# Performance work log

Hardware: AMD Instinct MI355X
Metric: run time of the kernel (lower is better)

The kernel has to match this reference:

```python
import jax, jax.numpy as jnp
import numpy as np

# Dimensions inferred from the module (few-shot reweighted YOLOv2 region loss)
B, C, NA, NCPA = 64, 20, 5, 1          # batch, base classes, anchors, classes-per-anchor
H, W = 19, 19                           # feature map (608 input / stride 32)
T = 50                                  # cfg.max_boxes
THRESH = 0.6
COORD_SCALE = 1.0
CLASS_SCALE = 1.0
NB = B * C                              # per-class 'image' rows, as in the torch code
A4 = NA * H * W
EPS = 1e-12
BCE_EPS = 1e-7
ANCHORS = [[1.3221, 1.73145], [3.19275, 4.00944], [5.05587, 8.09892], [9.47112, 4.84053], [11.2364, 10.0071]]


def iou_xywh(x1, y1, w1, h1, x2, y2, w2, h2):
    # center-size IoU, matches darknet bbox_iou(x1y1x2y2=False)
    l = jnp.maximum(x1 - w1 * 0.5, x2 - w2 * 0.5)
    r = jnp.minimum(x1 + w1 * 0.5, x2 + w2 * 0.5)
    t = jnp.maximum(y1 - h1 * 0.5, y2 - h2 * 0.5)
    b = jnp.minimum(y1 + h1 * 0.5, y2 + h2 * 0.5)
    inter = jnp.clip(r - l, 0.0) * jnp.clip(b - t, 0.0)
    union = w1 * h1 + w2 * h2 - inter
    return inter / jnp.maximum(union, EPS)


def setup_inputs() -> dict:
    key = jax.random.key(0)
    k1, k2, k3, k4 = jax.random.split(key, 4)
    output = jax.random.normal(k1, (NB, NA * (5 + NCPA), H, W), jnp.float32) * 0.5
    # target rows: [cls, x, y, w, h] * T, coords in (0,1); x kept > 0 so all boxes are 'valid'
    cls_ids = jax.random.randint(k2, (B, C, T), 0, C).astype(jnp.float32)
    xy = jax.random.uniform(k3, (B, C, T, 2), minval=0.05, maxval=0.95)
    wh = jax.random.uniform(k4, (B, C, T, 2), minval=0.05, maxval=0.5)
    target = jnp.concatenate([cls_ids[..., None], xy, wh], axis=-1).reshape(B, C, T * 5)
    anchors = jnp.asarray(ANCHORS, jnp.float32)
    return {"output": output, "target": target, "anchors": anchors}


def _forward(output, target, anchors):
    target = jax.lax.stop_gradient(target)
    anchors = jax.lax.stop_gradient(anchors)
    out5 = output.reshape(NB, NA, 5 + NCPA, H, W)
    x = jax.nn.sigmoid(out5[:, :, 0])
    y = jax.nn.sigmoid(out5[:, :, 1])
    w = out5[:, :, 2]
    h = out5[:, :, 3]
    conf = jax.nn.sigmoid(out5[:, :, 4])
    # class logits regrouped to original batch: (B*NA*H*W, C)
    cls = out5[:, :, 5:5 + NCPA].reshape(NB, NA, H, W)
    cls_logits = cls.reshape(B, C, NA * H * W).transpose(0, 2, 1).reshape(-1, C)
    # decode pred boxes (detached, mirroring torch's use of .data)
    grid_x = jnp.arange(W, dtype=jnp.float32)[None, None, None, :]
    grid_y = jnp.arange(H, dtype=jnp.float32)[None, None, :, None]
    aw = anchors[:, 0][None, :, None, None]
    ah = anchors[:, 1][None, :, None, None]
    px = jax.lax.stop_gradient(x) + grid_x
    py = jax.lax.stop_gradient(y) + grid_y
    pw = jnp.exp(jax.lax.stop_gradient(w)) * aw
    ph = jnp.exp(jax.lax.stop_gradient(h)) * ah
    # ground-truth boxes per row
    tgt = target.reshape(NB, T, 5)
    cls_t = tgt[:, :, 0]
    gx = tgt[:, :, 1] * W
    gy = tgt[:, :, 2] * H
    gw = tgt[:, :, 3] * W
    gh = tgt[:, :, 4] * H
    # 'break on first zero x' semantics
    valid = jnp.cumprod((tgt[:, :, 1] != 0).astype(jnp.int32), axis=1) > 0
    # stage 1: zero conf_mask where any gt IoU > thresh (scan over T to avoid (NB,T,A4) blowup)
    pxf = px.reshape(NB, A4); pyf = py.reshape(NB, A4)
    pwf = pw.reshape(NB, A4); phf = ph.reshape(NB, A4)

    def iou_step(ci, xs):
        gxt, gyt, gwt, ght, vt = xs
        iou = iou_xywh(pxf, pyf, pwf, phf, gxt[:, None], gyt[:, None], gwt[:, None], ght[:, None])
        return jnp.maximum(ci, jnp.where(vt[:, None], iou, 0.0)), None

    cur_ious, _ = jax.lax.scan(iou_step, jnp.zeros((NB, A4), jnp.float32), (gx.T, gy.T, gw.T, gh.T, valid.T))
    conf_mask0 = jnp.where(cur_ious.reshape(NB, NA, H, W) > THRESH, 0.0, 1.0)
    # best anchor per gt by wh-only IoU
    inter = jnp.minimum(gw[..., None], anchors[:, 0]) * jnp.minimum(gh[..., None], anchors[:, 1])
    union = gw[..., None] * gh[..., None] + anchors[:, 0] * anchors[:, 1] - inter
    best_n = jnp.argmax(inter / jnp.maximum(union, EPS), axis=-1).astype(jnp.int32)  # (NB,T)
    gi = gx.astype(jnp.int32)
    gj = gy.astype(jnp.int32)
    # stage 2: ordered scatter of targets (later boxes overwrite earlier, as in the torch loops)
    binds = jnp.arange(NB)
    z = jnp.zeros((NB, NA, H, W), jnp.float32)
    # seen < 12800 branch: tx=ty=0.5, tw=th=0, coord_mask=1
    carry0 = (jnp.ones_like(z), z, conf_mask0, jnp.full_like(z, 0.5), jnp.full_like(z, 0.5), z, z, z, z)

    def tgt_step(carry, xs):
        cm, clm, cfm, tx, ty, tw, th, tconf, tcls = carry
        gxt, gyt, gwt, ght, bn, git, gjt, vt, ct = xs
        idx = (binds, bn, gjt, git)

        def upd(arr, val):
            return arr.at[idx].set(jnp.where(vt, val, arr[idx]))

        aw_b = anchors[bn, 0]
        ah_b = anchors[bn, 1]
        iou = iou_xywh(gxt, gyt, gwt, ght, px[idx], py[idx], pw[idx], ph[idx])
        cm = upd(cm, 1.0)
        clm = upd(clm, 1.0)
        cfm = upd(cfm, 1.0)
        tx = upd(tx, gxt - git.astype(jnp.float32))
        ty = upd(ty, gyt - gjt.astype(jnp.float32))
        tw = upd(tw, jnp.log(jnp.maximum(gwt, EPS) / aw_b))
        th = upd(th, jnp.log(jnp.maximum(ght, EPS) / ah_b))
        tconf = upd(tconf, iou)
        tcls = upd(tcls, ct)
        return (cm, clm, cfm, tx, ty, tw, th, tconf, tcls), None

    xs = (gx.T, gy.T, gw.T, gh.T, best_n.T, gi.T, gj.T, valid.T, cls_t.T)
    (coord_mask, cls_mask, conf_mask, tx, ty, tw, th, tconf, tcls), _ = jax.lax.scan(tgt_step, carry0, xs)
    # regroup per-class rows back to original batch (neg_ratio='full' -> counts[i] == C)
    cm_grp = cls_mask.reshape(B, C, NA, H, W).sum(axis=1)
    tcls_grp = tcls.reshape(B, C, NA, H, W).sum(axis=1)
    sel = (cm_grp == 1.0).reshape(-1)           # exclude colliding cells
    labels = tcls_grp.reshape(-1).astype(jnp.int32)

    def bce_mean(p, t):
        p = jnp.clip(p, BCE_EPS, 1.0 - BCE_EPS)
        return jnp.mean(-(t * jnp.log(p) + (1.0 - t) * jnp.log(1.0 - p)))

    loss_x = COORD_SCALE * bce_mean(x * coord_mask, tx * coord_mask)
    loss_y = COORD_SCALE * bce_mean(y * coord_mask, ty * coord_mask)
    loss_w = COORD_SCALE * 0.5 * jnp.mean((w * coord_mask - tw * coord_mask) ** 2)
    loss_h = COORD_SCALE * 0.5 * jnp.mean((h * coord_mask - th * coord_mask) ** 2)
    loss_conf = 0.5 * jnp.mean((conf * conf_mask - tconf * conf_mask) ** 2)
    logp = jax.nn.log_softmax(cls_logits, axis=-1)
    nll = -jnp.take_along_axis(logp, labels[:, None], axis=1)[:, 0]
    nsel = jnp.maximum(jnp.sum(sel.astype(jnp.float32)), 1.0)
    loss_cls = CLASS_SCALE * jnp.sum(jnp.where(sel, nll, 0.0)) / nsel
    return loss_x + loss_y + loss_w + loss_h + loss_conf + loss_cls


def reference(output, target, anchors):
    return _forward(output, target, anchors)
```

## Files before the change

kernel.cpp:

```cpp
#include <hip/hip_runtime.h>
#include <math.h>

constexpr int cB   = 64;
constexpr int cC   = 20;
constexpr int cNA  = 5;
constexpr int cH   = 19;
constexpr int cW   = 19;
constexpr int cT   = 50;
constexpr int cNB  = cB * cC;
constexpr int cHW  = cH * cW;
constexpr int cA4  = cNA * cHW;
constexpr int cCH  = cNA * 6;
constexpr long cNTOT = (long)cNB * cA4;
constexpr int cCLS_BLOCKS = cB * cNA * 2;

__device__ __constant__ float cAW[cNA]   = {1.3221f, 3.19275f, 5.05587f, 9.47112f, 11.2364f};
__device__ __constant__ float cAH[cNA]   = {1.73145f, 4.00944f, 8.09892f, 4.84053f, 10.0071f};
__device__ __constant__ float cAREA[cNA] = {2.28930345f, 12.80114796f, 40.94706183f, 45.84455262f, 112.44377644f};
__device__ __constant__ float cLNAW[cNA] = {0.27920469f, 1.16088088f, 1.62060702f, 2.24822684f, 2.41915174f};
__device__ __constant__ float cLNAH[cNA] = {0.54896100f, 1.38865236f, 2.09173157f, 1.57701337f, 2.30329495f};

constexpr int ACC_BANKS = 64;
constexpr size_t OFF_CNT = 2560;
constexpr size_t OFF_ROW = 4096;
constexpr size_t ZERO_BYTES = OFF_ROW + (size_t)cB * cA4 * 4;

__device__ __forceinline__ float fexp(float x) {
    return __builtin_amdgcn_exp2f(x * 1.4426950408889634f);
}
__device__ __forceinline__ float flog(float x) {
    return __builtin_amdgcn_logf(x) * 0.6931471805599453f;
}
__device__ __forceinline__ float frcp(float x) { return __builtin_amdgcn_rcpf(x); }
__device__ __forceinline__ float fsigmoid(float x) { return frcp(1.0f + fexp(-x)); }

typedef _Float16 h2 __attribute__((ext_vector_type(2)));
union HU { unsigned u; h2 h; };
__device__ __forceinline__ unsigned splat2(float v) {
    HU x; _Float16 f = (_Float16)v; x.h[0] = f; x.h[1] = f; return x.u;
}
constexpr float cS = 1.2649110640673518f;

__launch_bounds__(512, 8)
__global__ void k_main(const float* __restrict__ outp, const float* __restrict__ target,
                       int* __restrict__ rowenc, double* __restrict__ acc) {
    __shared__ int s_win[cA4];
    __shared__ int s_tc[cT];
    __shared__ __align__(16) unsigned s_box[cT][8];
    __shared__ __align__(16) float4 s_gt[cT];
    __shared__ double s_red[3][8];
    const int tid = threadIdx.x;
    const int nb  = blockIdx.x;
    const int b_  = nb / cC;
    const int c_  = nb - b_ * cC;
    const float* obase = outp + (size_t)nb * (cCH * cHW);

    for (int k = tid; k < cA4; k += 512) s_win[k] = -1;
    __syncthreads();

    if (tid < 64) {
        const int t = tid;
        float xr = 1.f, yr = 0.f, wr = 0.f, hr = 0.f;
        if (t < cT) {
            const float* tg = target + (size_t)nb * (cT * 5) + t * 5;
            xr = tg[1]; yr = tg[2]; wr = tg[3]; hr = tg[4];
        }
        unsigned long long nz = __ballot(xr != 0.0f);
        if (t < cT) {
            unsigned long long below = (2ull << t) - 1ull;
            bool valid = ((~nz) & below) == 0ull;
            float gx = xr * (float)cW, gy = yr * (float)cH;
            float gw = wr * (float)cW, gh = hr * (float)cH;
            s_gt[t] = make_float4(gx, gy, gw, gh);
            if (valid) {
                s_box[t][0] = splat2(cS * (gx - 0.5f * gw));
                s_box[t][1] = splat2(cS * (gx + 0.5f * gw));
                s_box[t][2] = splat2(cS * (gy - 0.5f * gh));
                s_box[t][3] = splat2(cS * (gy + 0.5f * gh));
                s_box[t][4] = splat2(-0.6f * (gw * gh));
                float garea = gw * gh;
                float best = -1.0f; int bn = 0;
                for (int n = 0; n < cNA; ++n) {
                    float inter = fminf(gw, cAW[n]) * fminf(gh, cAH[n]);
                    float uni   = garea + cAREA[n] - inter;
                    float r = inter / fmaxf(uni, 1e-12f);
                    if (r > best) { best = r; bn = n; }
                }
                int cell = bn * cHW + (int)gy * cW + (int)gx;
                s_tc[t] = cell;
                atomicMax(&s_win[cell], t);
            } else {
                s_box[t][0] = splat2(1e4f);  s_box[t][1] = splat2(-1e4f);
                s_box[t][2] = splat2(1e4f);  s_box[t][3] = splat2(-1e4f);
                s_box[t][4] = splat2(0.0f);
                s_tc[t] = -1;
            }
        }
    }
    __syncthreads();
    if (tid < cT) {
        int cell = s_tc[tid];
        if (cell >= 0 && s_win[cell] == tid)
            atomicAdd(&rowenc[b_ * cA4 + cell], (1 << 10) | (c_ * cT + tid));
    }

    h2 pl2[2], pr2[2], pt2[2], pb2[2], ov2[2], pa06h[2];
    float conf[4], tcf[4];
    unsigned wbits = 0;
    float bce = 0.0f, sq = 0.0f;
    const h2 z2 = { (_Float16)0.0f, (_Float16)0.0f };

    #pragma unroll
    for (int u = 0; u < 4; ++u) {
        int cell = tid + (u << 9);
        bool a_  = cell < cA4;
        int cc   = a_ ? cell : (cA4 - 1);
        int na   = cc / cHW;
        int rem  = cc - na * cHW;
        int j    = rem / cW;
        int i    = rem - j * cW;
        const float* ob = obase + (size_t)(na * 6) * cHW + rem;
        float xl = ob[0], yl = ob[cHW], wl = ob[2*cHW], hl = ob[3*cHW], cl = ob[4*cHW];
        float aw = cAW[na], ah = cAH[na];
        float x  = fsigmoid(xl), y = fsigmoid(yl), cf = fsigmoid(cl);
        float px = x + (float)i, py = y + (float)j;
        float pw = fexp(wl) * aw, ph = fexp(hl) * ah;
        float l0 = px - 0.5f*pw, r0 = px + 0.5f*pw;
        float t0 = py - 0.5f*ph, b0 = py + 0.5f*ph;
        float pa = pw * ph;
        int p = u >> 1, s = u & 1;
        pl2[p][s] = (_Float16)(cS * l0);  pr2[p][s] = (_Float16)(cS * r0);
        pt2[p][s] = (_Float16)(cS * t0);  pb2[p][s] = (_Float16)(cS * b0);
        pa06h[p][s] = (_Float16)(0.6f * pa);
        ov2[p][s] = (_Float16)0.0f;
        conf[u] = cf; tcf[u] = 0.0f;

        float tx = 0.5f, ty = 0.5f, tw = 0.0f, th = 0.0f;
        int wt = s_win[cc];
        bool wfl = (wt >= 0) && a_;
        if (wfl) {
            wbits |= (1u << u);
            float4 g = s_gt[wt];
            float gx = g.x, gy = g.y, gw = g.z, gh = g.w;
            tx = gx - (float)i; ty = gy - (float)j;
            tw = flog(fmaxf(gw, 1e-12f)) - cLNAW[na];
            th = flog(fmaxf(gh, 1e-12f)) - cLNAH[na];
            float iw = fminf(r0, gx + 0.5f*gw) - fmaxf(l0, gx - 0.5f*gw);
            float ih = fminf(b0, gy + 0.5f*gh) - fmaxf(t0, gy - 0.5f*gh);
            iw = fmaxf(iw, 0.0f); ih = fmaxf(ih, 0.0f);
            float inter = iw * ih;
            float uni   = gw*gh + pa - inter;
            tcf[u] = inter * frcp(fmaxf(uni, 1e-12f));
        }
        if (a_) {
            float pc = fminf(fmaxf(x, 1e-7f), 1.0f - 1e-7f);
            bce += -(tx * flog(pc) + (1.0f - tx) * flog(1.0f - pc));
            pc = fminf(fmaxf(y, 1e-7f), 1.0f - 1e-7f);
            bce += -(ty * flog(pc) + (1.0f - ty) * flog(1.0f - pc));
            float dw = wl - tw, dh = hl - th;
            sq += dw*dw + dh*dh;
        }
    }

    #pragma unroll 10
    for (int t = 0; t < cT; ++t) {
        uint4 bx = *(const uint4*)&s_box[t][0];
        unsigned gv = s_box[t][4];
        HU a, b, c, d, e;
        a.u = bx.x; b.u = bx.y; c.u = bx.z; d.u = bx.w; e.u = gv;
        #pragma unroll
        for (int p = 0; p < 2; ++p) {
            h2 iw = __builtin_elementwise_min(pr2[p], b.h) - __builtin_elementwise_max(pl2[p], a.h);
            h2 ih = __builtin_elementwise_min(pb2[p], d.h) - __builtin_elementwise_max(pt2[p], c.h);
            iw = __builtin_elementwise_max(iw, z2);
            ih = __builtin_elementwise_max(ih, z2);
            ov2[p] = __builtin_elementwise_max(ov2[p], iw * ih + e.h);
        }
    }

    float sc = 0.0f;
    #pragma unroll
    for (int u = 0; u < 4; ++u) {
        int cell = tid + (u << 9);
        if (cell >= cA4) continue;
        int p = u >> 1, s = u & 1;
        bool wfl  = (wbits >> u) & 1;
        bool over = ov2[p][s] > pa06h[p][s];
        float cm  = wfl ? 1.0f : (over ? 0.0f : 1.0f);
        float d   = (conf[u] - tcf[u]) * cm;
        sc += d * d;
    }

    double v0 = (double)bce, v1 = (double)sq, v2 = (double)sc;
    for (int off = 32; off > 0; off >>= 1) {
        v0 += __shfl_down(v0, off);
        v1 += __shfl_down(v1, off);
        v2 += __shfl_down(v2, off);
    }
    int lane = tid & 63, wid = tid >> 6;
    if (lane == 0) { s_red[0][wid] = v0; s_red[1][wid] = v1; s_red[2][wid] = v2; }
    __syncthreads();
    if (tid == 0) {
        double a0 = 0.0, a1 = 0.0, a2 = 0.0;
        #pragma unroll
        for (int w = 0; w < 8; ++w) { a0 += s_red[0][w]; a1 += s_red[1][w]; a2 += s_red[2][w]; }
        int bank = nb & (ACC_BANKS - 1);
        atomicAdd(&acc[0*ACC_BANKS + bank], a0);
        atomicAdd(&acc[1*ACC_BANKS + bank], a1);
        atomicAdd(&acc[2*ACC_BANKS + bank], a2);
    }
}

__launch_bounds__(192)
__global__ void k_cls(const float* __restrict__ outp, const float* __restrict__ target,
                      const int* __restrict__ rowenc, double* __restrict__ acc,
                      int* __restrict__ cnt, float* __restrict__ out) {
    __shared__ double s_red[2][3];
    __shared__ int s_last;
    const int tid  = threadIdx.x;
    const int blk  = blockIdx.x;
    const int b    = blk / (cNA * 2);
    const int r2   = blk - b * (cNA * 2);
    const int na   = r2 >> 1;
    const int half = r2 & 1;
    const int rem  = half * 192 + tid;
    double nll = 0.0, ns = 0.0;
    if (rem < cHW) {
        const float* ob = outp + ((size_t)(b * cC) * cCH + na * 6 + 5) * cHW + rem;
        float l[cC]; float m = -1e30f;
        #pragma unroll
        for (int c = 0; c < cC; ++c) {
            l[c] = ob[(size_t)c * (cCH * cHW)];
            m = fmaxf(m, l[c]);
        }
        float s = 0.0f;
        #pragma unroll
        for (int c = 0; c < cC; ++c) s += fexp(l[c] - m);
        float lse = m + flog(s);
        int v = rowenc[b * cA4 + na * cHW + rem];
        if ((v >> 10) == 1) {
            int payload = v & 1023;
            int selc = payload / cT;
            int selt = payload - selc * cT;
            int label = (int)target[((size_t)(b * cC + selc) * cT + selt) * 5];
            nll = (double)(lse - l[label]);
            ns  = 1.0;
        }
    }
    for (int off = 32; off > 0; off >>= 1) {
        nll += __shfl_down(nll, off);
        ns  += __shfl_down(ns, off);
    }
    int lane = tid & 63, wid = tid >> 6;
    if (lane == 0) { s_red[0][wid] = nll; s_red[1][wid] = ns; }
    __syncthreads();
    if (tid == 0) {
        double a0 = s_red[0][0] + s_red[0][1] + s_red[0][2];
        double a1 = s_red[1][0] + s_red[1][1] + s_red[1][2];
        int bank = blk & (ACC_BANKS - 1);
        atomicAdd(&acc[3*ACC_BANKS + bank], a0);
        atomicAdd(&acc[4*ACC_BANKS + bank], a1);
        __threadfence();
        s_last = (atomicAdd(cnt, 1) == cCLS_BLOCKS - 1);
    }
    __syncthreads();
    if (s_last && tid < 64) {
        __threadfence();
        double s[5];
        #pragma unroll
        for (int j = 0; j < 5; ++j) {
            double v = atomicAdd(&acc[j * ACC_BANKS + tid], 0.0);
            for (int off = 32; off > 0; off >>= 1) v += __shfl_down(v, off);
            s[j] = v;
        }
        if (tid == 0) {
            double Ninv = 1.0 / (double)cNTOT;
            double loss = s[0] * Ninv
                        + 0.5 * s[1] * Ninv
                        + 0.5 * s[2] * Ninv
                        + s[3] / fmax(s[4], 1.0);
            out[0] = (float)loss;
        }
    }
}

extern "C" void kernel_launch(void* const* d_in, const int* in_sizes, int n_in,
                              void* d_out, int out_size, void* d_ws, size_t ws_size,
                              hipStream_t stream) {
    const float* output = (const float*)d_in[0];
    const float* target = (const float*)d_in[1];
    char* ws = (char*)d_ws;
    double* acc    = (double*)ws;
    int*    cnt    = (int*)(ws + OFF_CNT);
    int*    rowenc = (int*)(ws + OFF_ROW);

    hipMemsetAsync(ws, 0, ZERO_BYTES, stream);

    k_main<<<cNB, 512, 0, stream>>>(output, target, rowenc, acc);
    k_cls<<<cCLS_BLOCKS, 192, 0, stream>>>(output, target, rowenc, acc, cnt, (float*)d_out);
}
```

Baseline: 133.8 us.

## Stage per-row output slab in LDS and halve block size to 256 threads

The main kernel now copies the whole 30x361 output slab for its row into shared memory with coalesced float2 loads, then reads the channel values from LDS. Blocks shrink to 256 threads, and each thread now handles 8 cells instead of 4, with the fp16 IoU loop widened to match. Inactive cells get sentinel boxes. The aim is better memory-level parallelism and more per-thread ILP. The cost is about 43KB of LDS per block, which lowers occupancy. The barrier between the s_win initialisation and the atomicMax writes is gone, which opens a possible race.

Result: slower. 136.7 us (+2.2%).

```diff
diff --git a/kernel.cpp b/kernel.cpp
--- a/kernel.cpp
+++ b/kernel.cpp
@@ -11,6 +11,7 @@
 constexpr int cHW  = cH * cW;
 constexpr int cA4  = cNA * cHW;
 constexpr int cCH  = cNA * 6;
+constexpr int cSLAB = cCH * cHW;
 constexpr long cNTOT = (long)cNB * cA4;
 constexpr int cCLS_BLOCKS = cB * cNA * 2;
 
@@ -41,22 +42,43 @@
 }
 constexpr float cS = 1.2649110640673518f;
 
-__launch_bounds__(512, 8)
+__launch_bounds__(256)
 __global__ void k_main(const float* __restrict__ outp, const float* __restrict__ target,
                        int* __restrict__ rowenc, double* __restrict__ acc) {
+    __shared__ float s_slab[cSLAB];
     __shared__ int s_win[cA4];
     __shared__ int s_tc[cT];
     __shared__ __align__(16) unsigned s_box[cT][8];
     __shared__ __align__(16) float4 s_gt[cT];
-    __shared__ double s_red[3][8];
+    __shared__ double s_red[3][4];
     const int tid = threadIdx.x;
     const int nb  = blockIdx.x;
     const int b_  = nb / cC;
     const int c_  = nb - b_ * cC;
-    const float* obase = outp + (size_t)nb * (cCH * cHW);
-
-    for (int k = tid; k < cA4; k += 512) s_win[k] = -1;
-    __syncthreads();
+    const float2* g2 = (const float2*)(outp + (size_t)nb * cSLAB);
+    float2* s2 = (float2*)s_slab;
+
+    {
+        float2 v[11];
+        #pragma unroll
+        for (int k = 0; k < 11; ++k) {
+            int idx = tid + k * 256;
+            v[k] = g2[idx];
+        }
+        #pragma unroll
+        for (int k = 0; k < 11; ++k) s2[tid + k * 256] = v[k];
+        #pragma unroll
+        for (int k = 0; k < 11; ++k) {
+            int idx = tid + (k + 11) * 256;
+            v[k] = (idx < 5415) ? g2[idx] : make_float2(0.f, 0.f);
+        }
+        #pragma unroll
+        for (int k = 0; k < 11; ++k) {
+            int idx = tid + (k + 11) * 256;
+            if (idx < 5415) s2[idx] = v[k];
+        }
+    }
+    for (int k = tid; k < cA4; k += 256) s_win[k] = -1;
 
     if (tid < 64) {
         const int t = tid;
@@ -104,23 +126,23 @@
             atomicAdd(&rowenc[b_ * cA4 + cell], (1 << 10) | (c_ * cT + tid));
     }
 
-    h2 pl2[2], pr2[2], pt2[2], pb2[2], ov2[2], pa06h[2];
-    float conf[4], tcf[4];
+    h2 pl2[4], pr2[4], pt2[4], pb2[4], ov2[4], pa06h[4];
+    float conf[8], tcf[8];
     unsigned wbits = 0;
     float bce = 0.0f, sq = 0.0f;
     const h2 z2 = { (_Float16)0.0f, (_Float16)0.0f };
 
     #pragma unroll
-    for (int u = 0; u < 4; ++u) {
-        int cell = tid + (u << 9);
+    for (int u = 0; u < 8; ++u) {
+        int cell = tid + (u << 8);
         bool a_  = cell < cA4;
         int cc   = a_ ? cell : (cA4 - 1);
         int na   = cc / cHW;
         int rem  = cc - na * cHW;
         int j    = rem / cW;
         int i    = rem - j * cW;
-        const float* ob = obase + (size_t)(na * 6) * cHW + rem;
-        float xl = ob[0], yl = ob[cHW], wl = ob[2*cHW], hl = ob[3*cHW], cl = ob[4*cHW];
+        const float* sb = s_slab + (size_t)(na * 6) * cHW + rem;
+        float xl = sb[0], yl = sb[cHW], wl = sb[2*cHW], hl = sb[3*cHW], cl = sb[4*cHW];
         float aw = cAW[na], ah = cAH[na];
         float x  = fsigmoid(xl), y = fsigmoid(yl), cf = fsigmoid(cl);
         float px = x + (float)i, py = y + (float)j;
@@ -129,8 +151,13 @@
         float t0 = py - 0.5f*ph, b0 = py + 0.5f*ph;
         float pa = pw * ph;
         int p = u >> 1, s = u & 1;
-        pl2[p][s] = (_Float16)(cS * l0);  pr2[p][s] = (_Float16)(cS * r0);
-        pt2[p][s] = (_Float16)(cS * t0);  pb2[p][s] = (_Float16)(cS * b0);
+        if (a_) {
+            pl2[p][s] = (_Float16)(cS * l0);  pr2[p][s] = (_Float16)(cS * r0);
+            pt2[p][s] = (_Float16)(cS * t0);  pb2[p][s] = (_Float16)(cS * b0);
+        } else {
+            pl2[p][s] = (_Float16)1e4f;  pr2[p][s] = (_Float16)(-1e4f);
+            pt2[p][s] = (_Float16)1e4f;  pb2[p][s] = (_Float16)(-1e4f);
+        }
         pa06h[p][s] = (_Float16)(0.6f * pa);
         ov2[p][s] = (_Float16)0.0f;
         conf[u] = cf; tcf[u] = 0.0f;
@@ -169,7 +196,7 @@
         HU a, b, c, d, e;
         a.u = bx.x; b.u = bx.y; c.u = bx.z; d.u = bx.w; e.u = gv;
         #pragma unroll
-        for (int p = 0; p < 2; ++p) {
+        for (int p = 0; p < 4; ++p) {
             h2 iw = __builtin_elementwise_min(pr2[p], b.h) - __builtin_elementwise_max(pl2[p], a.h);
             h2 ih = __builtin_elementwise_min(pb2[p], d.h) - __builtin_elementwise_max(pt2[p], c.h);
             iw = __builtin_elementwise_max(iw, z2);
@@ -180,8 +207,8 @@
 
     float sc = 0.0f;
     #pragma unroll
-    for (int u = 0; u < 4; ++u) {
-        int cell = tid + (u << 9);
+    for (int u = 0; u < 8; ++u) {
+        int cell = tid + (u << 8);
         if (cell >= cA4) continue;
         int p = u >> 1, s = u & 1;
         bool wfl  = (wbits >> u) & 1;
@@ -201,9 +228,9 @@
     if (lane == 0) { s_red[0][wid] = v0; s_red[1][wid] = v1; s_red[2][wid] = v2; }
     __syncthreads();
     if (tid == 0) {
-        double a0 = 0.0, a1 = 0.0, a2 = 0.0;
-        #pragma unroll
-        for (int w = 0; w < 8; ++w) { a0 += s_red[0][w]; a1 += s_red[1][w]; a2 += s_red[2][w]; }
+        double a0 = s_red[0][0] + s_red[0][1] + s_red[0][2] + s_red[0][3];
+        double a1 = s_red[1][0] + s_red[1][1] + s_red[1][2] + s_red[1][3];
+        double a2 = s_red[2][0] + s_red[2][1] + s_red[2][2] + s_red[2][3];
         int bank = nb & (ACC_BANKS - 1);
         atomicAdd(&acc[0*ACC_BANKS + bank], a0);
         atomicAdd(&acc[1*ACC_BANKS + bank], a1);
@@ -296,6 +323,6 @@
 
     hipMemsetAsync(ws, 0, ZERO_BYTES, stream);
 
-    k_main<<<cNB, 512, 0, stream>>>(output, target, rowenc, acc);
+    k_main<<<cNB, 256, 0, stream>>>(output, target, rowenc, acc);
     k_cls<<<cCLS_BLOCKS, 192, 0, stream>>>(output, target, rowenc, acc, cnt, (float*)d_out);
 }
```

## Split each row across two 256-thread blocks and precompute GT boxes in a prep kernel

Applied to the files above, without the earlier changes.

Adds a small kernel that packs the per-row ground-truth boxes into fp16 pairs in workspace, so the main kernel reads them from global memory instead of building them in LDS. Each 1805-cell row is now handled by two 256-thread blocks, each covering half the cells. This gives twice as many smaller blocks and replaces the shared-memory box reads with uniform global loads. The cost is an extra kernel launch, both halves redoing the s_win/target setup, and the box loop now depending on global (cached) loads.

After: 138.3 us. 1.03x slower.

```diff
diff --git a/kernel.cpp b/kernel.cpp
--- a/kernel.cpp
+++ b/kernel.cpp
@@ -21,9 +21,10 @@
 __device__ __constant__ float cLNAH[cNA] = {0.54896100f, 1.38865236f, 2.09173157f, 1.57701337f, 2.30329495f};
 
 constexpr int ACC_BANKS = 64;
-constexpr size_t OFF_CNT = 2560;
-constexpr size_t OFF_ROW = 4096;
+constexpr size_t OFF_CNT  = 2560;
+constexpr size_t OFF_ROW  = 4096;
 constexpr size_t ZERO_BYTES = OFF_ROW + (size_t)cB * cA4 * 4;
+constexpr size_t OFF_SBOX = ZERO_BYTES;
 
 __device__ __forceinline__ float fexp(float x) {
     return __builtin_amdgcn_exp2f(x * 1.4426950408889634f);
@@ -41,21 +42,54 @@
 }
 constexpr float cS = 1.2649110640673518f;
 
-__launch_bounds__(512, 8)
+__global__ void k_prep_box(const float* __restrict__ target, unsigned* __restrict__ sbox) {
+    const int nb = blockIdx.x;
+    const int t  = threadIdx.x;
+    float xr = 1.f, yr = 0.f, wr = 0.f, hr = 0.f;
+    if (t < cT) {
+        const float* tg = target + (size_t)nb * (cT * 5) + t * 5;
+        xr = tg[1]; yr = tg[2]; wr = tg[3]; hr = tg[4];
+    }
+    unsigned long long nz = __ballot(xr != 0.0f);
+    if (t < cT) {
+        unsigned long long below = (2ull << t) - 1ull;
+        bool valid = ((~nz) & below) == 0ull;
+        uint4 w0, w1;
+        if (valid) {
+            float gx = xr * (float)cW, gy = yr * (float)cH;
+            float gw = wr * (float)cW, gh = hr * (float)cH;
+            w0 = make_uint4(splat2(cS * (gx - 0.5f * gw)),
+                            splat2(cS * (gx + 0.5f * gw)),
+                            splat2(cS * (gy - 0.5f * gh)),
+                            splat2(cS * (gy + 0.5f * gh)));
+            w1 = make_uint4(splat2(-0.6f * (gw * gh)), 0u, 0u, 0u);
+        } else {
+            w0 = make_uint4(splat2(1e4f), splat2(-1e4f), splat2(1e4f), splat2(-1e4f));
+            w1 = make_uint4(splat2(0.0f), 0u, 0u, 0u);
+        }
+        uint4* dst = (uint4*)(sbox + (size_t)nb * 400 + t * 8);
+        dst[0] = w0;
+        dst[1] = w1;
+    }
+}
+
+__launch_bounds__(256)
 __global__ void k_main(const float* __restrict__ outp, const float* __restrict__ target,
+                       const unsigned* __restrict__ sbox,
                        int* __restrict__ rowenc, double* __restrict__ acc) {
     __shared__ int s_win[cA4];
     __shared__ int s_tc[cT];
-    __shared__ __align__(16) unsigned s_box[cT][8];
     __shared__ __align__(16) float4 s_gt[cT];
-    __shared__ double s_red[3][8];
-    const int tid = threadIdx.x;
-    const int nb  = blockIdx.x;
-    const int b_  = nb / cC;
-    const int c_  = nb - b_ * cC;
+    __shared__ double s_red[3][4];
+    const int tid  = threadIdx.x;
+    const int nb   = blockIdx.x >> 1;
+    const int half = blockIdx.x & 1;
+    const int base = (half << 10) + tid;
+    const int b_   = nb / cC;
+    const int c_   = nb - b_ * cC;
     const float* obase = outp + (size_t)nb * (cCH * cHW);
 
-    for (int k = tid; k < cA4; k += 512) s_win[k] = -1;
+    for (int k = tid; k < cA4; k += 256) s_win[k] = -1;
     __syncthreads();
 
     if (tid < 64) {
@@ -73,11 +107,6 @@
             float gw = wr * (float)cW, gh = hr * (float)cH;
             s_gt[t] = make_float4(gx, gy, gw, gh);
             if (valid) {
-                s_box[t][0] = splat2(cS * (gx - 0.5f * gw));
-                s_box[t][1] = splat2(cS * (gx + 0.5f * gw));
-                s_box[t][2] = splat2(cS * (gy - 0.5f * gh));
-                s_box[t][3] = splat2(cS * (gy + 0.5f * gh));
-                s_box[t][4] = splat2(-0.6f * (gw * gh));
                 float garea = gw * gh;
                 float best = -1.0f; int bn = 0;
                 for (int n = 0; n < cNA; ++n) {
@@ -90,15 +119,12 @@
                 s_tc[t] = cell;
                 atomicMax(&s_win[cell], t);
             } else {
-                s_box[t][0] = splat2(1e4f);  s_box[t][1] = splat2(-1e4f);
-                s_box[t][2] = splat2(1e4f);  s_box[t][3] = splat2(-1e4f);
-                s_box[t][4] = splat2(0.0f);
                 s_tc[t] = -1;
             }
         }
     }
     __syncthreads();
-    if (tid < cT) {
+    if (half == 0 && tid < cT) {
         int cell = s_tc[tid];
         if (cell >= 0 && s_win[cell] == tid)
             atomicAdd(&rowenc[b_ * cA4 + cell], (1 << 10) | (c_ * cT + tid));
@@ -112,7 +138,7 @@
 
     #pragma unroll
     for (int u = 0; u < 4; ++u) {
-        int cell = tid + (u << 9);
+        int cell = base + (u << 8);
         bool a_  = cell < cA4;
         int cc   = a_ ? cell : (cA4 - 1);
         int na   = cc / cHW;
@@ -129,8 +155,13 @@
         float t0 = py - 0.5f*ph, b0 = py + 0.5f*ph;
         float pa = pw * ph;
         int p = u >> 1, s = u & 1;
-        pl2[p][s] = (_Float16)(cS * l0);  pr2[p][s] = (_Float16)(cS * r0);
-        pt2[p][s] = (_Float16)(cS * t0);  pb2[p][s] = (_Float16)(cS * b0);
+        if (a_) {
+            pl2[p][s] = (_Float16)(cS * l0);  pr2[p][s] = (_Float16)(cS * r0);
+            pt2[p][s] = (_Float16)(cS * t0);  pb2[p][s] = (_Float16)(cS * b0);
+        } else {
+            pl2[p][s] = (_Float16)1e4f;  pr2[p][s] = (_Float16)(-1e4f);
+            pt2[p][s] = (_Float16)1e4f;  pb2[p][s] = (_Float16)(-1e4f);
+        }
         pa06h[p][s] = (_Float16)(0.6f * pa);
         ov2[p][s] = (_Float16)0.0f;
         conf[u] = cf; tcf[u] = 0.0f;
@@ -162,12 +193,13 @@
         }
     }
 
+    const unsigned* tb32 = sbox + (size_t)nb * 400;
     #pragma unroll 10
     for (int t = 0; t < cT; ++t) {
-        uint4 bx = *(const uint4*)&s_box[t][0];
-        unsigned gv = s_box[t][4];
         HU a, b, c, d, e;
-        a.u = bx.x; b.u = bx.y; c.u = bx.z; d.u = bx.w; e.u = gv;
+        a.u = tb32[t*8 + 0]; b.u = tb32[t*8 + 1];
+        c.u = tb32[t*8 + 2]; d.u = tb32[t*8 + 3];
+        e.u = tb32[t*8 + 4];
         #pragma unroll
         for (int p = 0; p < 2; ++p) {
             h2 iw = __builtin_elementwise_min(pr2[p], b.h) - __builtin_elementwise_max(pl2[p], a.h);
@@ -181,7 +213,7 @@
     float sc = 0.0f;
     #pragma unroll
     for (int u = 0; u < 4; ++u) {
-        int cell = tid + (u << 9);
+        int cell = base + (u << 8);
         if (cell >= cA4) continue;
         int p = u >> 1, s = u & 1;
         bool wfl  = (wbits >> u) & 1;
@@ -201,10 +233,10 @@
     if (lane == 0) { s_red[0][wid] = v0; s_red[1][wid] = v1; s_red[2][wid] = v2; }
     __syncthreads();
     if (tid == 0) {
-        double a0 = 0.0, a1 = 0.0, a2 = 0.0;
-        #pragma unroll
-        for (int w = 0; w < 8; ++w) { a0 += s_red[0][w]; a1 += s_red[1][w]; a2 += s_red[2][w]; }
-        int bank = nb & (ACC_BANKS - 1);
+        double a0 = s_red[0][0] + s_red[0][1] + s_red[0][2] + s_red[0][3];
+        double a1 = s_red[1][0] + s_red[1][1] + s_red[1][2] + s_red[1][3];
+        double a2 = s_red[2][0] + s_red[2][1] + s_red[2][2] + s_red[2][3];
+        int bank = blockIdx.x & (ACC_BANKS - 1);
         atomicAdd(&acc[0*ACC_BANKS + bank], a0);
         atomicAdd(&acc[1*ACC_BANKS + bank], a1);
         atomicAdd(&acc[2*ACC_BANKS + bank], a2);
@@ -290,12 +322,14 @@
     const float* output = (const float*)d_in[0];
     const float* target = (const float*)d_in[1];
     char* ws = (char*)d_ws;
-    double* acc    = (double*)ws;
-    int*    cnt    = (int*)(ws + OFF_CNT);
-    int*    rowenc = (int*)(ws + OFF_ROW);
+    double*   acc    = (double*)ws;
+    int*      cnt    = (int*)(ws + OFF_CNT);
+    int*      rowenc = (int*)(ws + OFF_ROW);
+    unsigned* sbox   = (unsigned*)(ws + OFF_SBOX);
 
     hipMemsetAsync(ws, 0, ZERO_BYTES, stream);
 
-    k_main<<<cNB, 512, 0, stream>>>(output, target, rowenc, acc);
+    k_prep_box<<<cNB, 64, 0, stream>>>(target, sbox);
+    k_main<<<cNB * 2, 256, 0, stream>>>(output, target, sbox, rowenc, acc);
     k_cls<<<cCLS_BLOCKS, 192, 0, stream>>>(output, target, rowenc, acc, cnt, (float*)d_out);
 }
```
